# Performance work log

Measured on AMD Instinct MI355X. Metric: run time of the kernel, lower is better.

## Reference

```python
import jax, jax.numpy as jnp
import numpy as np

EPS = 1e-5

def _layer_norm(t, w, b):
    m = jnp.mean(t, axis=-1, keepdims=True)
    v = jnp.var(t, axis=-1, keepdims=True)
    return (t - m) * jax.lax.rsqrt(v + EPS) * w + b

def setup_inputs() -> dict:
    key = jax.random.key(0)
    ks = jax.random.split(key, 9)
    B, N, C, H = 1, 512, 128, 128
    s = 0.02
    return {
        "x": jax.random.normal(ks[0], (B, N, N, C), dtype=jnp.float32),
        "norm_in_w": jax.random.normal(ks[1], (C,), dtype=jnp.float32) * s + 1.0,
        "norm_in_b": jax.random.normal(ks[2], (C,), dtype=jnp.float32) * s,
        "p_in_w": jax.random.normal(ks[3], (2 * H, C), dtype=jnp.float32) * s,
        "g_in_w": jax.random.normal(ks[4], (2 * H, C), dtype=jnp.float32) * s,
        "norm_out_w": jax.random.normal(ks[5], (H,), dtype=jnp.float32) * s + 1.0,
        "norm_out_b": jax.random.normal(ks[6], (H,), dtype=jnp.float32) * s,
        "p_out_w": jax.random.normal(ks[7], (C, H), dtype=jnp.float32) * s,
        "g_out_w": jax.random.normal(ks[8], (C, C), dtype=jnp.float32) * s,
    }

def reference(x, norm_in_w, norm_in_b, p_in_w, g_in_w,
              norm_out_w, norm_out_b, p_out_w, g_out_w):
    # ending=False ("outgoing edges" triangle multiplicative update)
    x_norm_in = _layer_norm(x, norm_in_w, norm_in_b)          # [B,N,N,C]
    p = x_norm_in @ p_in_w.T                                   # [B,N,N,2H]
    g = jax.nn.sigmoid(x_norm_in @ g_in_w.T)                   # [B,N,N,2H]
    h = p * g
    d = h.shape[-1] // 2
    a, b = h[..., :d], h[..., d:]                              # each [B,N,N,H]
    # ttnn permutes: a->(0,3,1,2)=[B,H,i,k], b->(0,3,2,1)=[B,H,k,j] with b[...,k,j]=x2[b,j,k,h]
    o = jnp.einsum('bikh,bjkh->bijh', a, b)                    # [B,N,N,H]
    o_norm = _layer_norm(o, norm_out_w, norm_out_b)
    p_out = o_norm @ p_out_w.T                                 # [B,N,N,C]
    g_out = jax.nn.sigmoid(x_norm_in @ g_out_w.T)              # [B,N,N,C]
    return p_out * g_out
```

## Files before the change

### kernel.cpp

```cpp
#include <hip/hip_runtime.h>
#include <hip/hip_bf16.h>
#include <stdint.h>

typedef unsigned short u16;
typedef __attribute__((ext_vector_type(8))) short short8;
typedef __attribute__((ext_vector_type(4))) float f32x4;

#define NSEQ 512
#define PLANE (NSEQ*NSEQ)
#define CH 128
#define MTOT ((size_t)NSEQ*NSEQ)

__device__ __forceinline__ u16 f2bf(float f){
  __hip_bfloat16 h = __float2bfloat16(f);
  return *reinterpret_cast<u16*>(&h);
}
__device__ __forceinline__ float bf2f(u16 u){
  union { unsigned int i; float f; } x; x.i = ((unsigned int)u) << 16; return x.f;
}
__device__ __forceinline__ float sigmf(float x){ return 1.0f/(1.0f + __expf(-x)); }

__device__ __forceinline__ void ldg_lds16(const void* g, void* l){
  __builtin_amdgcn_global_load_lds((const __attribute__((address_space(1))) void*)g,
                                   (__attribute__((address_space(3))) void*)l, 16, 0, 0);
}

__global__ __launch_bounds__(256) void k1_lnin(const float* __restrict__ x,
        const float* __restrict__ w, const float* __restrict__ b,
        u16* __restrict__ xn){
  int row  = blockIdx.x*4 + (threadIdx.x>>6);
  int lane = threadIdx.x & 63;
  const float* xr = x + (size_t)row*CH;
  float2 v = *reinterpret_cast<const float2*>(&xr[lane*2]);
  float s  = v.x + v.y;
  float s2 = v.x*v.x + v.y*v.y;
  #pragma unroll
  for(int off=32; off>0; off>>=1){ s += __shfl_xor(s, off); s2 += __shfl_xor(s2, off); }
  float mean = s*(1.f/CH);
  float rstd = rsqrtf(s2*(1.f/CH) - mean*mean + 1e-5f);
  float2 wv = *reinterpret_cast<const float2*>(&w[lane*2]);
  float2 bv = *reinterpret_cast<const float2*>(&b[lane*2]);
  ushort2 o;
  o.x = f2bf((v.x-mean)*rstd*wv.x + bv.x);
  o.y = f2bf((v.y-mean)*rstd*wv.y + bv.y);
  *reinterpret_cast<ushort2*>(&xn[(size_t)row*CH + lane*2]) = o;
}

__global__ __launch_bounds__(256) void kpack(const float* __restrict__ pw,
        const float* __restrict__ gw, const float* __restrict__ pow_,
        const float* __restrict__ gow, u16* wp, u16* wg, u16* wpo, u16* wgo){
  int i = blockIdx.x*256 + threadIdx.x;
  wp[i] = f2bf(pw[i]);
  wg[i] = f2bf(gw[i]);
  if(i < 128*128){ wpo[i] = f2bf(pow_[i]); wgo[i] = f2bf(gow[i]); }
}

__global__ __launch_bounds__(256) void k2_proj(const u16* __restrict__ xn,
        const u16* __restrict__ wp, const u16* __restrict__ wg,
        u16* __restrict__ apl, u16* __restrict__ bplanes){
  __shared__ u16 Al[128*64], Bp[64*64], Bg[64*64];
  const int tid = threadIdx.x, wave = tid>>6, lane = tid&63;
  const int r = lane&15, g = lane>>4;
  const int wm = (wave>>1)*64, wn = (wave&1)*32;
  const size_t m0 = (size_t)blockIdx.x*128;
  const int c0 = blockIdx.y*64;
  f32x4 accp[4][2] = {}; f32x4 accg[4][2] = {};
  for(int k0=0; k0<CH; k0+=64){
    __syncthreads();
    #pragma unroll
    for(int it=0; it<4; ++it)
      ldg_lds16(xn + (m0 + it*32 + (tid>>3))*CH + k0 + (tid&7)*8, &Al[it*2048 + wave*512]);
    #pragma unroll
    for(int it=0; it<2; ++it){
      ldg_lds16(wp + (size_t)(c0 + it*32 + (tid>>3))*CH + k0 + (tid&7)*8, &Bp[it*2048 + wave*512]);
      ldg_lds16(wg + (size_t)(c0 + it*32 + (tid>>3))*CH + k0 + (tid&7)*8, &Bg[it*2048 + wave*512]);
    }
    __syncthreads();
    #pragma unroll
    for(int kk=0; kk<2; ++kk){
      short8 af[4], bpf[2], bgf[2];
      #pragma unroll
      for(int mi=0;mi<4;++mi)
        af[mi] = *reinterpret_cast<const short8*>(&Al[(wm+mi*16+r)*64 + kk*32 + g*8]);
      #pragma unroll
      for(int ni=0;ni<2;++ni){
        bpf[ni] = *reinterpret_cast<const short8*>(&Bp[(wn+ni*16+r)*64 + kk*32 + g*8]);
        bgf[ni] = *reinterpret_cast<const short8*>(&Bg[(wn+ni*16+r)*64 + kk*32 + g*8]);
      }
      #pragma unroll
      for(int mi=0;mi<4;++mi)
        #pragma unroll
        for(int ni=0;ni<2;++ni){
          accp[mi][ni] = __builtin_amdgcn_mfma_f32_16x16x32_bf16(af[mi], bpf[ni], accp[mi][ni],0,0,0);
          accg[mi][ni] = __builtin_amdgcn_mfma_f32_16x16x32_bf16(af[mi], bgf[ni], accg[mi][ni],0,0,0);
        }
    }
  }
  #pragma unroll
  for(int mi=0;mi<4;++mi)
    #pragma unroll
    for(int ni=0;ni<2;++ni){
      int c = c0 + wn + ni*16 + r;
      size_t m = m0 + wm + mi*16 + g*4;
      u16* plane = (c < CH) ? (apl + (size_t)c*MTOT) : (bplanes + (size_t)(c-CH)*MTOT);
      ushort4 pk;
      pk.x = f2bf(accp[mi][ni][0] * sigmf(accg[mi][ni][0]));
      pk.y = f2bf(accp[mi][ni][1] * sigmf(accg[mi][ni][1]));
      pk.z = f2bf(accp[mi][ni][2] * sigmf(accg[mi][ni][2]));
      pk.w = f2bf(accp[mi][ni][3] * sigmf(accg[mi][ni][3]));
      *reinterpret_cast<ushort4*>(plane + m) = pk;
    }
}

__global__ __launch_bounds__(256) void k3_einsum(const u16* __restrict__ apl,
        const u16* __restrict__ bplanes, u16* __restrict__ opl){
  __shared__ u16 Al[128*64], Bl[128*64];
  const int tid = threadIdx.x, wave = tid>>6, lane = tid&63;
  const int r = lane&15, g = lane>>4;
  const int wm = (wave>>1)*64, wn = (wave&1)*64;
  const int h = blockIdx.y;
  const int i0 = (blockIdx.x>>2)*128, j0 = (blockIdx.x&3)*128;
  const u16* A = apl     + (size_t)h*MTOT;
  const u16* B = bplanes + (size_t)h*MTOT;
  u16* O = opl + (size_t)h*MTOT;
  f32x4 acc[4][4] = {};
  for(int k0=0; k0<NSEQ; k0+=64){
    __syncthreads();
    #pragma unroll
    for(int it=0; it<4; ++it){
      ldg_lds16(A + (size_t)(i0 + it*32 + (tid>>3))*NSEQ + k0 + (tid&7)*8, &Al[it*2048 + wave*512]);
      ldg_lds16(B + (size_t)(j0 + it*32 + (tid>>3))*NSEQ + k0 + (tid&7)*8, &Bl[it*2048 + wave*512]);
    }
    __syncthreads();
    #pragma unroll
    for(int kk=0; kk<2; ++kk){
      short8 af[4], bf[4];
      #pragma unroll
      for(int mi=0;mi<4;++mi)
        af[mi] = *reinterpret_cast<const short8*>(&Al[(wm+mi*16+r)*64 + kk*32 + g*8]);
      #pragma unroll
      for(int ni=0;ni<4;++ni)
        bf[ni] = *reinterpret_cast<const short8*>(&Bl[(wn+ni*16+r)*64 + kk*32 + g*8]);
      #pragma unroll
      for(int mi=0;mi<4;++mi)
        #pragma unroll
        for(int ni=0;ni<4;++ni)
          acc[mi][ni] = __builtin_amdgcn_mfma_f32_16x16x32_bf16(af[mi], bf[ni], acc[mi][ni],0,0,0);
    }
  }
  #pragma unroll
  for(int mi=0;mi<4;++mi)
    #pragma unroll
    for(int ni=0;ni<4;++ni){
      int ib = i0 + wm + mi*16 + g*4;
      int j  = j0 + wn + ni*16 + r;
      #pragma unroll
      for(int v=0;v<4;++v)
        O[(size_t)(ib+v)*NSEQ + j] = f2bf(acc[mi][ni][v]);
    }
}

__global__ __launch_bounds__(256) void k4a_lnout(const u16* __restrict__ opl,
        const float* __restrict__ w, const float* __restrict__ b,
        u16* __restrict__ onorm){
  __shared__ u16 S[128*136];
  const int tid = threadIdx.x;
  const int i = blockIdx.y, j0 = blockIdx.x*128;
  #pragma unroll
  for(int rep=0; rep<8; ++rep){
    int hh = rep*16 + (tid>>4), ck = tid&15;
    *reinterpret_cast<short8*>(&S[hh*136 + ck*8]) =
      *reinterpret_cast<const short8*>(opl + (size_t)hh*MTOT + (size_t)i*NSEQ + j0 + ck*8);
  }
  __syncthreads();
  if(tid < 128){
    int j = tid;
    float s=0.f, s2=0.f;
    for(int hh=0; hh<128; ++hh){
      float xv = bf2f(S[hh*136 + j]); s += xv; s2 += xv*xv;
    }
    float mean = s*(1.f/128.f);
    float rstd = rsqrtf(s2*(1.f/128.f) - mean*mean + 1e-5f);
    u16* dst = onorm + ((size_t)i*NSEQ + j0 + j)*CH;
    for(int h0=0; h0<128; h0+=8){
      short8 pk;
      #pragma unroll
      for(int t=0;t<8;++t){
        int hh = h0+t;
        float xv = bf2f(S[hh*136 + j]);
        pk[t] = (short)f2bf((xv-mean)*rstd*w[hh] + b[hh]);
      }
      *reinterpret_cast<short8*>(&dst[h0]) = pk;
    }
  }
}

__global__ __launch_bounds__(256) void k4b_out(const u16* __restrict__ onorm,
        const u16* __restrict__ xn, const u16* __restrict__ wpo,
        const u16* __restrict__ wgo, float* __restrict__ out){
  __shared__ u16 A1[128*64], A2[128*64], B1[64*64], B2[64*64];
  const int tid = threadIdx.x, wave = tid>>6, lane = tid&63;
  const int r = lane&15, g = lane>>4;
  const int wm = (wave>>1)*64, wn = (wave&1)*32;
  const size_t m0 = (size_t)blockIdx.x*128;
  const int n0 = blockIdx.y*64;
  f32x4 accp[4][2] = {}; f32x4 accg[4][2] = {};
  for(int k0=0; k0<CH; k0+=64){
    __syncthreads();
    #pragma unroll
    for(int it=0; it<4; ++it){
      ldg_lds16(onorm + (m0 + it*32 + (tid>>3))*CH + k0 + (tid&7)*8, &A1[it*2048 + wave*512]);
      ldg_lds16(xn    + (m0 + it*32 + (tid>>3))*CH + k0 + (tid&7)*8, &A2[it*2048 + wave*512]);
    }
    #pragma unroll
    for(int it=0; it<2; ++it){
      ldg_lds16(wpo + (size_t)(n0 + it*32 + (tid>>3))*CH + k0 + (tid&7)*8, &B1[it*2048 + wave*512]);
      ldg_lds16(wgo + (size_t)(n0 + it*32 + (tid>>3))*CH + k0 + (tid&7)*8, &B2[it*2048 + wave*512]);
    }
    __syncthreads();
    #pragma unroll
    for(int kk=0; kk<2; ++kk){
      short8 a1f[4], a2f[4], b1f[2], b2f[2];
      #pragma unroll
      for(int mi=0;mi<4;++mi){
        a1f[mi] = *reinterpret_cast<const short8*>(&A1[(wm+mi*16+r)*64 + kk*32 + g*8]);
        a2f[mi] = *reinterpret_cast<const short8*>(&A2[(wm+mi*16+r)*64 + kk*32 + g*8]);
      }
      #pragma unroll
      for(int ni=0;ni<2;++ni){
        b1f[ni] = *reinterpret_cast<const short8*>(&B1[(wn+ni*16+r)*64 + kk*32 + g*8]);
        b2f[ni] = *reinterpret_cast<const short8*>(&B2[(wn+ni*16+r)*64 + kk*32 + g*8]);
      }
      #pragma unroll
      for(int mi=0;mi<4;++mi)
        #pragma unroll
        for(int ni=0;ni<2;++ni){
          accp[mi][ni] = __builtin_amdgcn_mfma_f32_16x16x32_bf16(a1f[mi], b1f[ni], accp[mi][ni],0,0,0);
          accg[mi][ni] = __builtin_amdgcn_mfma_f32_16x16x32_bf16(a2f[mi], b2f[ni], accg[mi][ni],0,0,0);
        }
    }
  }
  #pragma unroll
  for(int mi=0;mi<4;++mi)
    #pragma unroll
    for(int ni=0;ni<2;++ni){
      int n = n0 + wn + ni*16 + r;
      size_t m = m0 + wm + mi*16 + g*4;
      #pragma unroll
      for(int v=0;v<4;++v)
        out[(m+v)*CH + n] = accp[mi][ni][v] * sigmf(accg[mi][ni][v]);
    }
}

extern "C" void kernel_launch(void* const* d_in, const int* in_sizes, int n_in,
                              void* d_out, int out_size, void* d_ws, size_t ws_size,
                              hipStream_t stream){
  const float* x       = (const float*)d_in[0];
  const float* nw_in   = (const float*)d_in[1];
  const float* nb_in   = (const float*)d_in[2];
  const float* p_in_w  = (const float*)d_in[3];
  const float* g_in_w  = (const float*)d_in[4];
  const float* nw_out  = (const float*)d_in[5];
  const float* nb_out  = (const float*)d_in[6];
  const float* p_out_w = (const float*)d_in[7];
  const float* g_out_w = (const float*)d_in[8];
  float* out = (float*)d_out;

  const size_t SZ = MTOT*CH*sizeof(u16);
  char* ws = (char*)d_ws;
  u16* xn      = (u16*)ws;
  u16* apl     = (u16*)(ws + SZ);
  u16* bplanes = (u16*)(ws + 2*SZ);
  u16* wpb     = (u16*)(ws + 3*SZ);
  u16* wgb     = wpb + 256*128;
  u16* wpob    = wgb + 256*128;
  u16* wgob    = wpob + 128*128;
  u16* opl     = (u16*)d_out;
  u16* onorm   = apl;

  kpack <<<128, 256, 0, stream>>>(p_in_w, g_in_w, p_out_w, g_out_w, wpb, wgb, wpob, wgob);
  k1_lnin<<<65536, 256, 0, stream>>>(x, nw_in, nb_in, xn);
  k2_proj<<<dim3(2048,4), 256, 0, stream>>>(xn, wpb, wgb, apl, bplanes);
  k3_einsum<<<dim3(16,128), 256, 0, stream>>>(apl, bplanes, opl);
  k4a_lnout<<<dim3(4,512), 256, 0, stream>>>(opl, nw_out, nb_out, onorm);
  k4b_out<<<dim3(2048,2), 256, 0, stream>>>(onorm, xn, wpob, wgob, out);
}
```

Measured before the change: 490.7 us.

## Stage GEMM epilogues through LDS, remap block IDs per XCD, widen layernorm kernels

The projection, einsum and output GEMMs now stage their results in shared memory and write them out as coalesced 16-byte rows instead of scattered 2-byte or 8-byte stores. Block indices are remapped so that consecutive blocks on each of the eight XCDs share tiles and weights, which should improve L2 locality. The input layernorm uses float4 loads with 32 lanes per row and a grid-stride loop over rows, and the output layernorm handles two rows per block so all 256 threads do work. These changes add LDS traffic and extra barriers, and they raise the shared-memory footprint per block.

```diff
diff --git a/kernel.cpp b/kernel.cpp
--- a/kernel.cpp
+++ b/kernel.cpp
@@ -7,7 +7,6 @@
 typedef __attribute__((ext_vector_type(4))) float f32x4;
 
 #define NSEQ 512
-#define PLANE (NSEQ*NSEQ)
 #define CH 128
 #define MTOT ((size_t)NSEQ*NSEQ)
 
@@ -28,22 +27,25 @@
 __global__ __launch_bounds__(256) void k1_lnin(const float* __restrict__ x,
         const float* __restrict__ w, const float* __restrict__ b,
         u16* __restrict__ xn){
-  int row  = blockIdx.x*4 + (threadIdx.x>>6);
-  int lane = threadIdx.x & 63;
-  const float* xr = x + (size_t)row*CH;
-  float2 v = *reinterpret_cast<const float2*>(&xr[lane*2]);
-  float s  = v.x + v.y;
-  float s2 = v.x*v.x + v.y*v.y;
-  #pragma unroll
-  for(int off=32; off>0; off>>=1){ s += __shfl_xor(s, off); s2 += __shfl_xor(s2, off); }
-  float mean = s*(1.f/CH);
-  float rstd = rsqrtf(s2*(1.f/CH) - mean*mean + 1e-5f);
-  float2 wv = *reinterpret_cast<const float2*>(&w[lane*2]);
-  float2 bv = *reinterpret_cast<const float2*>(&b[lane*2]);
-  ushort2 o;
-  o.x = f2bf((v.x-mean)*rstd*wv.x + bv.x);
-  o.y = f2bf((v.y-mean)*rstd*wv.y + bv.y);
-  *reinterpret_cast<ushort2*>(&xn[(size_t)row*CH + lane*2]) = o;
+  const int l32 = threadIdx.x & 31;
+  const float4 wv = *reinterpret_cast<const float4*>(&w[l32*4]);
+  const float4 bv = *reinterpret_cast<const float4*>(&b[l32*4]);
+  for(int rp=0; rp<8; ++rp){
+    size_t row = ((size_t)rp*4096 + blockIdx.x)*8 + (threadIdx.x>>5);
+    float4 v = *reinterpret_cast<const float4*>(&x[row*CH + l32*4]);
+    float s  = v.x+v.y+v.z+v.w;
+    float s2 = v.x*v.x + v.y*v.y + v.z*v.z + v.w*v.w;
+    #pragma unroll
+    for(int off=16; off>0; off>>=1){ s += __shfl_xor(s, off); s2 += __shfl_xor(s2, off); }
+    float mean = s*(1.f/CH);
+    float rstd = rsqrtf(s2*(1.f/CH) - mean*mean + 1e-5f);
+    ushort4 o;
+    o.x = f2bf((v.x-mean)*rstd*wv.x + bv.x);
+    o.y = f2bf((v.y-mean)*rstd*wv.y + bv.y);
+    o.z = f2bf((v.z-mean)*rstd*wv.z + bv.z);
+    o.w = f2bf((v.w-mean)*rstd*wv.w + bv.w);
+    *reinterpret_cast<ushort4*>(&xn[row*CH + l32*4]) = o;
+  }
 }
 
 __global__ __launch_bounds__(256) void kpack(const float* __restrict__ pw,
@@ -58,12 +60,16 @@
 __global__ __launch_bounds__(256) void k2_proj(const u16* __restrict__ xn,
         const u16* __restrict__ wp, const u16* __restrict__ wg,
         u16* __restrict__ apl, u16* __restrict__ bplanes){
-  __shared__ u16 Al[128*64], Bp[64*64], Bg[64*64];
+  __shared__ __align__(16) u16 SM[16384];
+  u16* Al = SM; u16* Bp = SM + 8192; u16* Bg = SM + 12288;
   const int tid = threadIdx.x, wave = tid>>6, lane = tid&63;
   const int r = lane&15, g = lane>>4;
   const int wm = (wave>>1)*64, wn = (wave&1)*32;
-  const size_t m0 = (size_t)blockIdx.x*128;
-  const int c0 = blockIdx.y*64;
+  const int bid = blockIdx.x;
+  const int l   = (bid&7)*1024 + (bid>>3);
+  const int y   = l&3;
+  const size_t m0 = (size_t)(l>>2)*128;
+  const int c0 = y*64;
   f32x4 accp[4][2] = {}; f32x4 accg[4][2] = {};
   for(int k0=0; k0<CH; k0+=64){
     __syncthreads();
@@ -96,30 +102,43 @@
         }
     }
   }
+  __syncthreads();
   #pragma unroll
   for(int mi=0;mi<4;++mi)
     #pragma unroll
     for(int ni=0;ni<2;++ni){
-      int c = c0 + wn + ni*16 + r;
-      size_t m = m0 + wm + mi*16 + g*4;
-      u16* plane = (c < CH) ? (apl + (size_t)c*MTOT) : (bplanes + (size_t)(c-CH)*MTOT);
+      int cl = wn + ni*16 + r;
+      int ml = wm + mi*16 + g*4;
       ushort4 pk;
       pk.x = f2bf(accp[mi][ni][0] * sigmf(accg[mi][ni][0]));
       pk.y = f2bf(accp[mi][ni][1] * sigmf(accg[mi][ni][1]));
       pk.z = f2bf(accp[mi][ni][2] * sigmf(accg[mi][ni][2]));
       pk.w = f2bf(accp[mi][ni][3] * sigmf(accg[mi][ni][3]));
-      *reinterpret_cast<ushort4*>(plane + m) = pk;
-    }
+      *reinterpret_cast<ushort4*>(&SM[cl*136 + ml]) = pk;
+    }
+  __syncthreads();
+  #pragma unroll
+  for(int e=0;e<4;++e){
+    int idx = e*256 + tid;
+    int c = idx>>4, chk = idx&15;
+    int cg = c0 + c;
+    u16* plane = (cg < CH) ? (apl + (size_t)cg*MTOT) : (bplanes + (size_t)(cg-CH)*MTOT);
+    *reinterpret_cast<short8*>(plane + m0 + chk*8) =
+      *reinterpret_cast<const short8*>(&SM[c*136 + chk*8]);
+  }
 }
 
 __global__ __launch_bounds__(256) void k3_einsum(const u16* __restrict__ apl,
         const u16* __restrict__ bplanes, u16* __restrict__ opl){
-  __shared__ u16 Al[128*64], Bl[128*64];
+  __shared__ __align__(16) u16 SM[17408];
+  u16* Al = SM; u16* Bl = SM + 8192;
   const int tid = threadIdx.x, wave = tid>>6, lane = tid&63;
   const int r = lane&15, g = lane>>4;
   const int wm = (wave>>1)*64, wn = (wave&1)*64;
-  const int h = blockIdx.y;
-  const int i0 = (blockIdx.x>>2)*128, j0 = (blockIdx.x&3)*128;
+  const int bid = blockIdx.x;
+  const int l   = (bid&7)*256 + (bid>>3);
+  const int h   = l>>4, ij = l&15;
+  const int i0  = (ij>>2)*128, j0 = (ij&3)*128;
   const u16* A = apl     + (size_t)h*MTOT;
   const u16* B = bplanes + (size_t)h*MTOT;
   u16* O = opl + (size_t)h*MTOT;
@@ -148,46 +167,57 @@
           acc[mi][ni] = __builtin_amdgcn_mfma_f32_16x16x32_bf16(af[mi], bf[ni], acc[mi][ni],0,0,0);
     }
   }
+  __syncthreads();
   #pragma unroll
   for(int mi=0;mi<4;++mi)
     #pragma unroll
     for(int ni=0;ni<4;++ni){
-      int ib = i0 + wm + mi*16 + g*4;
-      int j  = j0 + wn + ni*16 + r;
+      int row = wm + mi*16 + g*4;
+      int col = wn + ni*16 + r;
       #pragma unroll
       for(int v=0;v<4;++v)
-        O[(size_t)(ib+v)*NSEQ + j] = f2bf(acc[mi][ni][v]);
-    }
+        SM[(row+v)*136 + col] = f2bf(acc[mi][ni][v]);
+    }
+  __syncthreads();
+  #pragma unroll
+  for(int e=0;e<8;++e){
+    int idx = e*256 + tid;
+    int row = idx>>4, chk = idx&15;
+    *reinterpret_cast<short8*>(O + (size_t)(i0+row)*NSEQ + j0 + chk*8) =
+      *reinterpret_cast<const short8*>(&SM[row*136 + chk*8]);
+  }
 }
 
 __global__ __launch_bounds__(256) void k4a_lnout(const u16* __restrict__ opl,
         const float* __restrict__ w, const float* __restrict__ b,
         u16* __restrict__ onorm){
-  __shared__ u16 S[128*136];
+  __shared__ __align__(16) u16 S[2*128*144];
   const int tid = threadIdx.x;
-  const int i = blockIdx.y, j0 = blockIdx.x*128;
-  #pragma unroll
-  for(int rep=0; rep<8; ++rep){
-    int hh = rep*16 + (tid>>4), ck = tid&15;
-    *reinterpret_cast<short8*>(&S[hh*136 + ck*8]) =
-      *reinterpret_cast<const short8*>(opl + (size_t)hh*MTOT + (size_t)i*NSEQ + j0 + ck*8);
-  }
-  __syncthreads();
-  if(tid < 128){
-    int j = tid;
+  const int i = blockIdx.y*2, j0 = blockIdx.x*128;
+  #pragma unroll
+  for(int rep=0; rep<16; ++rep){
+    int half = rep>>3, rr = rep&7;
+    int hh = rr*16 + (tid>>4), ck = tid&15;
+    *reinterpret_cast<short8*>(&S[half*18432 + hh*144 + ck*8]) =
+      *reinterpret_cast<const short8*>(opl + (size_t)hh*MTOT + (size_t)(i+half)*NSEQ + j0 + ck*8);
+  }
+  __syncthreads();
+  {
+    int j = tid&127, half = tid>>7;
+    const u16* Sb = &S[half*18432];
     float s=0.f, s2=0.f;
     for(int hh=0; hh<128; ++hh){
-      float xv = bf2f(S[hh*136 + j]); s += xv; s2 += xv*xv;
+      float xv = bf2f(Sb[hh*144 + j]); s += xv; s2 += xv*xv;
     }
     float mean = s*(1.f/128.f);
     float rstd = rsqrtf(s2*(1.f/128.f) - mean*mean + 1e-5f);
-    u16* dst = onorm + ((size_t)i*NSEQ + j0 + j)*CH;
+    u16* dst = onorm + ((size_t)(i+half)*NSEQ + j0 + j)*CH;
     for(int h0=0; h0<128; h0+=8){
       short8 pk;
       #pragma unroll
       for(int t=0;t<8;++t){
         int hh = h0+t;
-        float xv = bf2f(S[hh*136 + j]);
+        float xv = bf2f(Sb[hh*144 + j]);
         pk[t] = (short)f2bf((xv-mean)*rstd*w[hh] + b[hh]);
       }
       *reinterpret_cast<short8*>(&dst[h0]) = pk;
@@ -198,12 +228,17 @@
 __global__ __launch_bounds__(256) void k4b_out(const u16* __restrict__ onorm,
         const u16* __restrict__ xn, const u16* __restrict__ wpo,
         const u16* __restrict__ wgo, float* __restrict__ out){
-  __shared__ u16 A1[128*64], A2[128*64], B1[64*64], B2[64*64];
+  __shared__ __align__(16) u16 SM[24576];
+  u16* A1 = SM; u16* A2 = SM + 8192; u16* B1 = SM + 16384; u16* B2 = SM + 20480;
+  float* E = (float*)SM;
   const int tid = threadIdx.x, wave = tid>>6, lane = tid&63;
   const int r = lane&15, g = lane>>4;
   const int wm = (wave>>1)*64, wn = (wave&1)*32;
-  const size_t m0 = (size_t)blockIdx.x*128;
-  const int n0 = blockIdx.y*64;
+  const int bid = blockIdx.x;
+  const int l   = (bid&7)*512 + (bid>>3);
+  const int y   = l&1;
+  const size_t m0 = (size_t)(l>>1)*128;
+  const int n0 = y*64;
   f32x4 accp[4][2] = {}; f32x4 accg[4][2] = {};
   for(int k0=0; k0<CH; k0+=64){
     __syncthreads();
@@ -240,16 +275,25 @@
         }
     }
   }
+  __syncthreads();
   #pragma unroll
   for(int mi=0;mi<4;++mi)
     #pragma unroll
     for(int ni=0;ni<2;++ni){
-      int n = n0 + wn + ni*16 + r;
-      size_t m = m0 + wm + mi*16 + g*4;
+      int row = wm + mi*16 + g*4;
+      int col = wn + ni*16 + r;
       #pragma unroll
       for(int v=0;v<4;++v)
-        out[(m+v)*CH + n] = accp[mi][ni][v] * sigmf(accg[mi][ni][v]);
-    }
+        E[(row+v)*68 + col] = accp[mi][ni][v] * sigmf(accg[mi][ni][v]);
+    }
+  __syncthreads();
+  #pragma unroll
+  for(int e=0;e<8;++e){
+    int idx = e*256 + tid;
+    int row = idx>>4, chk = idx&15;
+    *reinterpret_cast<float4*>(out + (m0+row)*CH + n0 + chk*4) =
+      *reinterpret_cast<const float4*>(&E[row*68 + chk*4]);
+  }
 }
 
 extern "C" void kernel_launch(void* const* d_in, const int* in_sizes, int n_in,
@@ -278,10 +322,10 @@
   u16* opl     = (u16*)d_out;
   u16* onorm   = apl;
 
-  kpack <<<128, 256, 0, stream>>>(p_in_w, g_in_w, p_out_w, g_out_w, wpb, wgb, wpob, wgob);
-  k1_lnin<<<65536, 256, 0, stream>>>(x, nw_in, nb_in, xn);
-  k2_proj<<<dim3(2048,4), 256, 0, stream>>>(xn, wpb, wgb, apl, bplanes);
-  k3_einsum<<<dim3(16,128), 256, 0, stream>>>(apl, bplanes, opl);
-  k4a_lnout<<<dim3(4,512), 256, 0, stream>>>(opl, nw_out, nb_out, onorm);
-  k4b_out<<<dim3(2048,2), 256, 0, stream>>>(onorm, xn, wpob, wgob, out);
-}
+  kpack  <<<128, 256, 0, stream>>>(p_in_w, g_in_w, p_out_w, g_out_w, wpb, wgb, wpob, wgob);
+  k1_lnin<<<4096, 256, 0, stream>>>(x, nw_in, nb_in, xn);
+  k2_proj<<<8192, 256, 0, stream>>>(xn, wpb, wgb, apl, bplanes);
+  k3_einsum<<<2048, 256, 0, stream>>>(apl, bplanes, opl);
+  k4a_lnout<<<dim3(4,256), 256, 0, stream>>>(opl, nw_out, nb_out, onorm);
+  k4b_out<<<4096, 256, 0, stream>>>(onorm, xn, wpob, wgob, out);
+}
```

New measurement: 476.2 us. 1.03x faster.
